# Performance work log

Hardware: AMD Instinct MI355X
Metric: run time of the kernel (lower is better)

The kernel has to match this reference:

```python
import jax, jax.numpy as jnp
import numpy as np

BETA = 0.25
N_EMBED = 1024
DIM = 256


def setup_inputs() -> dict:
    key = jax.random.key(0)
    k1, k2 = jax.random.split(key)
    z = jax.random.normal(k1, (8, DIM, 64, 64), dtype=jnp.float32)
    # matches nn.Embedding init: uniform(-1/n_embed, 1/n_embed)
    codebook = jax.random.uniform(
        k2, (N_EMBED, DIM), dtype=jnp.float32,
        minval=-1.0 / N_EMBED, maxval=1.0 / N_EMBED)
    return {"z": z, "codebook": codebook}


def reference(z, codebook):
    B, C, H, W = z.shape
    sg = jax.lax.stop_gradient
    zp = jnp.transpose(z, (0, 2, 3, 1))          # [B,H,W,C]
    zf = zp.reshape(-1, C)                        # [N,C], N = B*H*W
    # squared euclidean distances: ||z||^2 + ||e||^2 - 2 z.e
    d = (jnp.sum(zf * zf, axis=1, keepdims=True)
         + jnp.sum(codebook * codebook, axis=1)
         - 2.0 * zf @ codebook.T)                 # [N, n_embed]
    idx = jnp.argmin(d, axis=1)                   # [N]
    # one-hot @ codebook in the original is just an index gather
    z_q = codebook[idx].reshape(zp.shape)         # [B,H,W,C]
    loss = (BETA * jnp.mean((sg(z_q) - zp) ** 2)
            + jnp.mean((z_q - sg(zp)) ** 2))
    z_q_st = zp + sg(z_q - zp)                    # straight-through estimator
    z_q_out = jnp.transpose(z_q_st, (0, 3, 1, 2))  # back to NCHW
    return z_q_out, loss, idx.reshape(B, H, W)
```

## Files before the change

### kernel.cpp

```cpp
#include <hip/hip_runtime.h>
#include <hip/hip_fp16.h>

#define NELEM 8388608
#define M_GAP 6e-4f
#define SCORE_SCALE (-1.0f / 512.0f)

typedef _Float16 f16x8 __attribute__((ext_vector_type(8)));
typedef short s16x8 __attribute__((ext_vector_type(8)));
typedef float f32x4 __attribute__((ext_vector_type(4)));

__device__ __forceinline__ unsigned short bf16r(float f) {
  unsigned u = __float_as_uint(f);
  return (unsigned short)((u + 0x7fffu + ((u >> 16) & 1u)) >> 16);
}
__device__ __forceinline__ float bf16f(unsigned short h) {
  return __uint_as_float(((unsigned)h) << 16);
}

__device__ __forceinline__ float pw128_sq(const float* p, int s) {
  float r[8];
#pragma unroll
  for (int j = 0; j < 8; ++j) { float v = p[j * s]; r[j] = __fmul_rn(v, v); }
#pragma unroll
  for (int i = 8; i < 128; i += 8) {
#pragma unroll
    for (int j = 0; j < 8; ++j) {
      float v = p[(i + j) * s];
      r[j] = __fadd_rn(r[j], __fmul_rn(v, v));
    }
  }
  return __fadd_rn(__fadd_rn(__fadd_rn(r[0], r[1]), __fadd_rn(r[2], r[3])),
                   __fadd_rn(__fadd_rn(r[4], r[5]), __fadd_rn(r[6], r[7])));
}
__device__ __forceinline__ float np_sumsq256(const float* p, int s) {
  return __fadd_rn(pw128_sq(p, s), pw128_sq(p + 128 * s, s));
}

__global__ __launch_bounds__(256)
void vq_prep(const float* __restrict__ cb, unsigned short* __restrict__ cbimg,
             float* __restrict__ cbT, float* __restrict__ Bsg,
             unsigned* __restrict__ cnt, float* __restrict__ loss) {
  int gid = blockIdx.x * 256 + threadIdx.x;
  if (gid == 0) { *cnt = 0u; *loss = 0.0f; }
  int j = gid >> 2, qt = gid & 3;
  const float4* row4 = reinterpret_cast<const float4*>(cb + (size_t)j * 256 + qt * 64);
  int T = j >> 4, jj = j & 15;
#pragma unroll
  for (int m8 = 0; m8 < 8; ++m8) {
    int c0 = qt * 64 + m8 * 8;
    int kk = c0 >> 5, lk = (c0 >> 3) & 3;
    float4 va = row4[m8 * 2];
    float4 vb = row4[m8 * 2 + 1];
    float v[8] = {va.x, va.y, va.z, va.w, vb.x, vb.y, vb.z, vb.w};
    s16x8 hv;
#pragma unroll
    for (int q = 0; q < 8; ++q) {
      hv[q] = (short)__half_as_ushort(__float2half(v[q] * 1024.0f));
      cbT[(size_t)(c0 + q) * 1024 + j] = v[q];
    }
    *reinterpret_cast<s16x8*>(cbimg + (size_t)T * 4096 + kk * 512 + (lk * 16 + jj) * 8) = hv;
  }
  if (qt == 0) Bsg[j] = np_sumsq256(cb + (size_t)j * 256, 1);
}

#define VQ_STEP_PF(IT2, DO_PF)                                                 \
  {                                                                            \
    f32x4 acc[4];                                                              \
    _Pragma("unroll")                                                          \
    for (int rs = 0; rs < 4; ++rs) acc[rs] = (f32x4){0.f, 0.f, 0.f, 0.f};      \
    _Pragma("unroll")                                                          \
    for (int kk = 0; kk < 8; ++kk) {                                           \
      f16x8 bcur = ba[kk];                                                     \
      if (DO_PF)                                                               \
        ba[kk] = cimg2[(size_t)(wv * 16 + (IT2) + 1) * 512 + kk * 64 + lane];  \
      _Pragma("unroll")                                                        \
      for (int rs = 0; rs < 4; ++rs)                                           \
        acc[rs] = __builtin_amdgcn_mfma_f32_16x16x32_f16(ah[rs][kk], bcur,     \
                                                         acc[rs], 0, 0, 0);    \
    }                                                                          \
    int j = wv * 256 + (IT2) * 16 + l15;                                       \
    float Bj = BsL[j];                                                         \
    _Pragma("unroll")                                                          \
    for (int rs = 0; rs < 4; ++rs) {                                           \
      _Pragma("unroll")                                                        \
      for (int r = 0; r < 4; ++r) {                                            \
        float s = fmaf(SCORE_SCALE, acc[rs][r], Bj);                           \
        bool lt = s < b1v[rs][r];                                              \
        float other = lt ? b1v[rs][r] : s;                                     \
        b2v[rs][r] = fminf(b2v[rs][r], other);                                 \
        b1v[rs][r] = fminf(b1v[rs][r], s);                                     \
        b1i[rs][r] = lt ? j : b1i[rs][r];                                      \
      }                                                                        \
    }                                                                          \
  }

__global__ __launch_bounds__(256, 1)
void vq_fast(const float* __restrict__ z, const float* __restrict__ cb,
             const unsigned short* __restrict__ cbimg,
             const float* __restrict__ Bsg,
             float* __restrict__ zq, float* __restrict__ loss,
             float* __restrict__ idxo,
             unsigned* __restrict__ list, unsigned* __restrict__ cnt,
             float* __restrict__ zdump) {
  __shared__ __align__(16) unsigned char buf[58880];
  __shared__ float BsL[1024];
  __shared__ float part[32][36];
  __shared__ float rowA[64];
  __shared__ int bestj[64];
  __shared__ float bestd[64];
  __shared__ unsigned char flg[64];
  __shared__ float wred[4];
  __shared__ float cv1[4 * 64], cv2[4 * 64];
  __shared__ int ci1[4 * 64];

  const int t = threadIdx.x;
  const int bid = blockIdx.x;
  const int lane = t & 63;
  const int wv = t >> 6;
  const int l15 = lane & 15;
  const int lk = lane >> 4;

  const f16x8* cimg2 = reinterpret_cast<const f16x8*>(cbimg);
  float* zt = reinterpret_cast<float*>(buf);
  const float4* z4 = reinterpret_cast<const float4*>(
      z + (size_t)(bid >> 6) * 1048576 + (size_t)(bid & 63) * 64);

  f16x8 ba[8];
#pragma unroll
  for (int kk = 0; kk < 8; ++kk)
    ba[kk] = cimg2[(size_t)(wv * 16) * 512 + kk * 64 + lane];

  for (int i = t; i < 1024; i += 256) BsL[i] = Bsg[i];

  f16x8 ah[4][8];
#pragma unroll
  for (int hp = 0; hp < 2; ++hp) {
    float sq[4] = {0.f, 0.f, 0.f, 0.f};
#pragma unroll
    for (int i = 0; i < 8; ++i) {
      int idx = t + i * 256;
      int c = idx >> 3, w4p = idx & 7;
      float4 v = z4[(size_t)c * 1024 + hp * 8 + w4p];
      zt[c * 33 + w4p * 4 + 0] = v.x;
      zt[c * 33 + w4p * 4 + 1] = v.y;
      zt[c * 33 + w4p * 4 + 2] = v.z;
      zt[c * 33 + w4p * 4 + 3] = v.w;
      sq[0] += v.x * v.x; sq[1] += v.y * v.y;
      sq[2] += v.z * v.z; sq[3] += v.w * v.w;
    }
#pragma unroll
    for (int q = 0; q < 4; ++q) part[t >> 3][(t & 7) * 4 + q] = sq[q];
    __syncthreads();
    if (t < 32) {
      float s = 0.f;
#pragma unroll
      for (int g = 0; g < 32; ++g) s += part[g][t];
      rowA[hp * 32 + t] = s;
    }
#pragma unroll
    for (int rr2 = 0; rr2 < 2; ++rr2) {
      int lr = rr2 * 16 + l15;
#pragma unroll
      for (int kk = 0; kk < 8; ++kk)
#pragma unroll
        for (int m = 0; m < 8; ++m)
          ah[hp * 2 + rr2][kk][m] = (_Float16)zt[(kk * 32 + lk * 8 + m) * 33 + lr];
    }
    if (zdump) {
#pragma unroll
      for (int i = 0; i < 8; ++i) {
        int item = t + i * 256;
        int c4 = item & 63, rowp = item >> 6;
        float4 v = make_float4(zt[(c4 * 4 + 0) * 33 + rowp],
                               zt[(c4 * 4 + 1) * 33 + rowp],
                               zt[(c4 * 4 + 2) * 33 + rowp],
                               zt[(c4 * 4 + 3) * 33 + rowp]);
        *reinterpret_cast<float4*>(
            zdump + ((size_t)bid * 64 + hp * 32 + rowp) * 256 + c4 * 4) = v;
      }
    }
    __syncthreads();
  }

  float b1v[4][4], b2v[4][4];
  int b1i[4][4];
#pragma unroll
  for (int rs = 0; rs < 4; ++rs)
#pragma unroll
    for (int r = 0; r < 4; ++r) { b1v[rs][r] = 3.4e38f; b2v[rs][r] = 3.4e38f; b1i[rs][r] = 0; }

  for (int it = 0; it < 15; ++it) {
    VQ_STEP_PF(it, true);
  }
  VQ_STEP_PF(15, false);

#pragma unroll
  for (int mk = 1; mk < 16; mk <<= 1) {
#pragma unroll
    for (int rs = 0; rs < 4; ++rs)
#pragma unroll
      for (int r = 0; r < 4; ++r) {
        float ov1 = __shfl_xor(b1v[rs][r], mk, 64);
        float ov2 = __shfl_xor(b2v[rs][r], mk, 64);
        int oi1 = __shfl_xor(b1i[rs][r], mk, 64);
        bool lt = ov1 < b1v[rs][r];
        float hi = lt ? b1v[rs][r] : ov1;
        b2v[rs][r] = fminf(fminf(b2v[rs][r], ov2), hi);
        b1v[rs][r] = fminf(b1v[rs][r], ov1);
        b1i[rs][r] = lt ? oi1 : b1i[rs][r];
      }
  }
  if (l15 == 0) {
#pragma unroll
    for (int rs = 0; rs < 4; ++rs)
#pragma unroll
      for (int r = 0; r < 4; ++r) {
        int rr = rs * 16 + lk * 4 + r;
        cv1[wv * 64 + rr] = b1v[rs][r];
        cv2[wv * 64 + rr] = b2v[rs][r];
        ci1[wv * 64 + rr] = b1i[rs][r];
      }
  }
  __syncthreads();

  if (t < 64) {
    float v1 = cv1[t], v2 = cv2[t];
    int i1 = ci1[t];
#pragma unroll
    for (int w = 1; w < 4; ++w) {
      float u1 = cv1[w * 64 + t], u2 = cv2[w * 64 + t];
      int ui = ci1[w * 64 + t];
      if (u1 < v1) { v2 = fminf(v1, u2); v1 = u1; i1 = ui; }
      else v2 = fminf(v2, u1);
    }
    bestj[t] = i1;
    bestd[t] = v1;
    flg[t] = (v2 - v1 <= M_GAP) ? 1 : 0;
    int n = bid * 64 + t;
    idxo[n] = (float)i1;
    if (flg[t]) { unsigned pos = atomicAdd(cnt, 1u); list[pos] = (unsigned)n; }
  }
  __syncthreads();

  {
    float lv = (t < 64) ? (rowA[t] + bestd[t]) : 0.f;
#pragma unroll
    for (int off = 32; off > 0; off >>= 1) lv += __shfl_down(lv, off, 64);
    if (lane == 0) wred[wv] = lv;
  }
  __syncthreads();
  if (t == 0)
    atomicAdd(loss, (wred[0] + wred[1] + wred[2] + wred[3]) * (1.25f / (float)NELEM));

  f32x4* ldsF4 = reinterpret_cast<f32x4*>(buf);
  const float* ldsF = reinterpret_cast<const float*>(buf);
  const float4* cb4 = reinterpret_cast<const float4*>(cb);
  float* zqb = zq + (size_t)(bid >> 6) * 1048576 + (size_t)(bid & 63) * 64;
  for (int hp = 0; hp < 2; ++hp) {
    __syncthreads();
#pragma unroll
    for (int i = 0; i < 8; ++i) {
      int item = t + i * 256;
      int rr = item >> 6, cc = item & 63;
      float4 v = cb4[(size_t)bestj[hp * 32 + rr] * 64 + cc];
      ldsF4[rr * 64 + (cc ^ ((rr >> 2) & 7))] = (f32x4){v.x, v.y, v.z, v.w};
    }
    __syncthreads();
#pragma unroll
    for (int i = 0; i < 8; ++i) {
      int item = t + i * 256;
      int w4p = item & 7, c = item >> 3;
      float ov[4];
#pragma unroll
      for (int q = 0; q < 4; ++q) {
        int rr = w4p * 4 + q;
        ov[q] = ldsF[(rr * 64 + ((c >> 2) ^ ((rr >> 2) & 7))) * 4 + (c & 3)];
      }
      *reinterpret_cast<float4*>(zqb + (size_t)c * 4096 + hp * 32 + w4p * 4) =
          make_float4(ov[0], ov[1], ov[2], ov[3]);
    }
  }
}

__global__ __launch_bounds__(256)
void vq_exact_fast(const float* __restrict__ zdump, const float* __restrict__ cbT,
                   const float* __restrict__ Bsg, const unsigned* __restrict__ list,
                   const unsigned* __restrict__ cnt, float* __restrict__ idxo) {
  __shared__ float zr[8][260];
  __shared__ float Anp[8];
  __shared__ float rv[256];
  __shared__ int ri[256];
  const int t = threadIdx.x;
  const unsigned K = *cnt;
  const float4* cbT4 = reinterpret_cast<const float4*>(cbT);
  const float4* zd4 = reinterpret_cast<const float4*>(zdump);

  for (unsigned g = blockIdx.x; g * 8 < K; g += gridDim.x) {
    int nrows = (int)min(8u, K - g * 8);
    __syncthreads();
#pragma unroll
    for (int i = 0; i < 2; ++i) {
      int idx = t + i * 256;
      int r = idx >> 6, c4 = idx & 63;
      if (r < nrows) {
        float4 v = zd4[(size_t)list[g * 8 + r] * 64 + c4];
        zr[r][c4 * 4 + 0] = v.x; zr[r][c4 * 4 + 1] = v.y;
        zr[r][c4 * 4 + 2] = v.z; zr[r][c4 * 4 + 3] = v.w;
      }
    }
    __syncthreads();
    if (t < nrows) Anp[t] = np_sumsq256(&zr[t][0], 1);
    __syncthreads();

    float acc[8][4];
#pragma unroll
    for (int r = 0; r < 8; ++r)
#pragma unroll
      for (int q = 0; q < 4; ++q) acc[r][q] = 0.f;
    for (int c = 0; c < 256; ++c) {
      float4 bv = cbT4[c * 256 + t];
#pragma unroll
      for (int r = 0; r < 8; ++r) {
        float zc = zr[r][c];
        acc[r][0] = fmaf(zc, bv.x, acc[r][0]);
        acc[r][1] = fmaf(zc, bv.y, acc[r][1]);
        acc[r][2] = fmaf(zc, bv.z, acc[r][2]);
        acc[r][3] = fmaf(zc, bv.w, acc[r][3]);
      }
    }
    for (int r = 0; r < nrows; ++r) {
      float A = Anp[r];
      float bvv = 3.4e38f;
      int bii = 0;
#pragma unroll
      for (int q = 0; q < 4; ++q) {
        int j = t * 4 + q;
        float dd = __fsub_rn(__fadd_rn(A, Bsg[j]), __fmul_rn(2.0f, acc[r][q]));
        if (dd < bvv) { bvv = dd; bii = j; }
      }
      rv[t] = bvv; ri[t] = bii;
      __syncthreads();
      for (int s2 = 128; s2 > 0; s2 >>= 1) {
        if (t < s2) {
          float v2 = rv[t + s2]; int i2 = ri[t + s2];
          if (v2 < rv[t] || (v2 == rv[t] && i2 < ri[t])) { rv[t] = v2; ri[t] = i2; }
        }
        __syncthreads();
      }
      if (t == 0) idxo[list[g * 8 + r]] = (float)ri[0];
      __syncthreads();
    }
  }
}

__global__ __launch_bounds__(256)
void vq_exact_scatter(const float* __restrict__ z, const float* __restrict__ cbT,
                      const float* __restrict__ Bsg, const unsigned* __restrict__ list,
                      const unsigned* __restrict__ cnt, float* __restrict__ idxo) {
  __shared__ float zr[8][260];
  __shared__ float Anp[8];
  __shared__ float rv[256];
  __shared__ int ri[256];
  const int t = threadIdx.x;
  const unsigned K = *cnt;
  const float4* cbT4 = reinterpret_cast<const float4*>(cbT);

  for (unsigned g = blockIdx.x; g * 8 < K; g += gridDim.x) {
    int nrows = (int)min(8u, K - g * 8);
    __syncthreads();
    {
      int r = t >> 5, l32 = t & 31;
      if (r < nrows) {
        int n = (int)list[g * 8 + r];
        int b = n >> 12, hw = n & 4095;
        const float* zb = z + (size_t)b * 1048576 + hw;
#pragma unroll
        for (int q = 0; q < 8; ++q) {
          int c = l32 * 8 + q;
          zr[r][c] = zb[(size_t)c * 4096];
        }
      }
    }
    __syncthreads();
    if (t < nrows) Anp[t] = np_sumsq256(&zr[t][0], 1);
    __syncthreads();
    float acc[8][4];
#pragma unroll
    for (int r = 0; r < 8; ++r)
#pragma unroll
      for (int q = 0; q < 4; ++q) acc[r][q] = 0.f;
    for (int c = 0; c < 256; ++c) {
      float4 bv = cbT4[c * 256 + t];
#pragma unroll
      for (int r = 0; r < 8; ++r) {
        float zc = zr[r][c];
        acc[r][0] = fmaf(zc, bv.x, acc[r][0]);
        acc[r][1] = fmaf(zc, bv.y, acc[r][1]);
        acc[r][2] = fmaf(zc, bv.z, acc[r][2]);
        acc[r][3] = fmaf(zc, bv.w, acc[r][3]);
      }
    }
    for (int r = 0; r < nrows; ++r) {
      float A = Anp[r];
      float bvv = 3.4e38f;
      int bii = 0;
#pragma unroll
      for (int q = 0; q < 4; ++q) {
        int j = t * 4 + q;
        float dd = __fsub_rn(__fadd_rn(A, Bsg[j]), __fmul_rn(2.0f, acc[r][q]));
        if (dd < bvv) { bvv = dd; bii = j; }
      }
      rv[t] = bvv; ri[t] = bii;
      __syncthreads();
      for (int s2 = 128; s2 > 0; s2 >>= 1) {
        if (t < s2) {
          float v2 = rv[t + s2]; int i2 = ri[t + s2];
          if (v2 < rv[t] || (v2 == rv[t] && i2 < ri[t])) { rv[t] = v2; ri[t] = i2; }
        }
        __syncthreads();
      }
      if (t == 0) idxo[list[g * 8 + r]] = (float)ri[0];
      __syncthreads();
    }
  }
}

__global__ __launch_bounds__(256)
void vq_ref(const float* __restrict__ z, const float* __restrict__ cb,
            float* __restrict__ zq, float* __restrict__ loss,
            float* __restrict__ idxo) {
  __shared__ __align__(16) float zt[256 * 64];
  __shared__ __align__(16) float cbt[256 * 64];
  __shared__ float As[64];
  __shared__ float Bs[64];
  __shared__ int bestj[64];
  __shared__ float cand_v[16 * 64];
  __shared__ int cand_i[16 * 64];
  __shared__ double wred[4];
  const int t = threadIdx.x;
  const int wg = t & 15, jg = t >> 4;
  const int bid = blockIdx.x;
  const int b = bid >> 6, h = bid & 63;
  const int n0 = bid * 64;
  const float4* z4 = reinterpret_cast<const float4*>(z + (size_t)b * 256 * 4096 + (size_t)h * 64);
  float4* zt4 = reinterpret_cast<float4*>(zt);
#pragma unroll
  for (int i = 0; i < 16; ++i) {
    int idx4 = t + i * 256;
    zt4[idx4] = z4[(size_t)(idx4 >> 4) * 1024 + (idx4 & 15)];
  }
  __syncthreads();
  if (t < 64) As[t] = np_sumsq256(zt + t, 64);
  float bv[4]; int bi[4];
#pragma unroll
  for (int a = 0; a < 4; ++a) { bv[a] = 3.4e38f; bi[a] = 0; }
  for (int p = 0; p < 16; ++p) {
    __syncthreads();
    const float4* cb4 = reinterpret_cast<const float4*>(cb) + (size_t)p * 64 * 64;
#pragma unroll
    for (int i = 0; i < 16; ++i) {
      int idx4 = t + i * 256;
      int jj = idx4 >> 6, c4 = idx4 & 63;
      float4 v = cb4[idx4];
      cbt[(c4 * 4 + 0) * 64 + jj] = v.x;
      cbt[(c4 * 4 + 1) * 64 + jj] = v.y;
      cbt[(c4 * 4 + 2) * 64 + jj] = v.z;
      cbt[(c4 * 4 + 3) * 64 + jj] = v.w;
    }
    __syncthreads();
    if (t < 64) Bs[t] = np_sumsq256(cbt + t, 64);
    float acc[4][4];
#pragma unroll
    for (int a = 0; a < 4; ++a)
#pragma unroll
      for (int u = 0; u < 4; ++u) acc[a][u] = 0.0f;
    const float4* ztp = reinterpret_cast<const float4*>(zt) + wg;
    const float4* cbp = reinterpret_cast<const float4*>(cbt) + jg;
#pragma unroll 4
    for (int c = 0; c < 256; ++c) {
      float4 zv = ztp[c * 16];
      float4 cv = cbp[c * 16];
      float za[4] = {zv.x, zv.y, zv.z, zv.w};
      float ca[4] = {cv.x, cv.y, cv.z, cv.w};
#pragma unroll
      for (int a = 0; a < 4; ++a)
#pragma unroll
        for (int u = 0; u < 4; ++u) acc[a][u] = fmaf(za[a], ca[u], acc[a][u]);
    }
    __syncthreads();
#pragma unroll
    for (int u = 0; u < 4; ++u) {
      int j = p * 64 + jg * 4 + u;
      float Bju = Bs[jg * 4 + u];
#pragma unroll
      for (int a = 0; a < 4; ++a) {
        float AB = __fadd_rn(As[wg * 4 + a], Bju);
        float dd = __fsub_rn(AB, __fmul_rn(2.0f, acc[a][u]));
        if (dd < bv[a]) { bv[a] = dd; bi[a] = j; }
      }
    }
  }
  __syncthreads();
#pragma unroll
  for (int a = 0; a < 4; ++a) {
    int w = wg * 4 + a;
    cand_v[jg * 64 + w] = bv[a];
    cand_i[jg * 64 + w] = bi[a];
  }
  __syncthreads();
  if (t < 64) {
    float v0 = cand_v[t]; int i0 = cand_i[t];
    for (int g = 1; g < 16; ++g) {
      float v = cand_v[g * 64 + t]; int ii = cand_i[g * 64 + t];
      if (v < v0 || (v == v0 && ii < i0)) { v0 = v; i0 = ii; }
    }
    bestj[t] = i0;
    idxo[n0 + t] = (float)i0;
  }
  __syncthreads();
  double lsum = 0.0;
  float* zqbase = zq + (size_t)b * 256 * 4096 + (size_t)h * 64;
  for (int i = 0; i < 64; ++i) {
    int idx = t + i * 256;
    int c = idx >> 6, w = idx & 63;
    float zvv = zt[c * 64 + w];
    float cvv = cb[(size_t)bestj[w] * 256 + c];
    zqbase[(size_t)c * 4096 + w] = cvv;
    double d = (double)cvv - (double)zvv;
    lsum += d * d;
  }
#pragma unroll
  for (int off = 32; off > 0; off >>= 1) lsum += __shfl_down(lsum, off, 64);
  if ((t & 63) == 0) wred[t >> 6] = lsum;
  __syncthreads();
  if (t == 0) {
    double tot = wred[0] + wred[1] + wred[2] + wred[3];
    atomicAdd(loss, (float)(tot * (1.25 / (double)NELEM)));
  }
}

extern "C" void kernel_launch(void* const* d_in, const int* in_sizes, int n_in,
                              void* d_out, int out_size, void* d_ws, size_t ws_size,
                              hipStream_t stream) {
  (void)in_sizes; (void)n_in; (void)out_size;
  const float* z = (const float*)d_in[0];
  const float* cb = (const float*)d_in[1];
  float* out = (float*)d_out;
  float* zq = out;
  float* loss = out + NELEM;
  float* idxo = out + NELEM + 1;
  if (ws_size < 1712128) {
    hipMemsetAsync(loss, 0, sizeof(float), stream);
    vq_ref<<<512, 256, 0, stream>>>(z, cb, zq, loss, idxo);
    return;
  }
  unsigned char* ws = (unsigned char*)d_ws;
  unsigned* cnt = (unsigned*)ws;
  float* Bsg = (float*)(ws + 1024);
  unsigned* list = (unsigned*)(ws + 8192);
  float* cbT = (float*)(ws + 139264);
  unsigned short* cbimg = (unsigned short*)(ws + 1187840);
  const bool have_dump = (ws_size >= 35651584);
  float* zdump = have_dump ? (float*)(ws + 2097152) : nullptr;
  vq_prep<<<16, 256, 0, stream>>>(cb, cbimg, cbT, Bsg, cnt, loss);
  vq_fast<<<512, 256, 0, stream>>>(z, cb, cbimg, Bsg, zq, loss, idxo, list, cnt, zdump);
  if (have_dump)
    vq_exact_fast<<<512, 256, 0, stream>>>(zdump, cbT, Bsg, list, cnt, idxo);
  else
    vq_exact_scatter<<<512, 256, 0, stream>>>(z, cbT, Bsg, list, cnt, idxo);
}
```

Measured before the change: 104.0 us.

## Track top-3 scores to resolve near-ties with a cheap two-candidate check

The fast fp16 MFMA pass now keeps the best three scores and the top two indices per row. Ambiguous rows whose third-best is clearly separated go to a new per-thread kernel that recomputes only the two candidate distances in fp32. Only rows with three-way near ties fall back to the full exact rescan over all 1024 codes. The scatter fallback is removed, the z dump is always written, and the smaller-workspace path now uses the reference kernel. The extra compare logic and registers in the hot loop may cost occupancy or issue slots, and there is one more kernel launch.

```diff
diff --git a/kernel.cpp b/kernel.cpp
--- a/kernel.cpp
+++ b/kernel.cpp
@@ -41,7 +41,7 @@
              float* __restrict__ cbT, float* __restrict__ Bsg,
              unsigned* __restrict__ cnt, float* __restrict__ loss) {
   int gid = blockIdx.x * 256 + threadIdx.x;
-  if (gid == 0) { *cnt = 0u; *loss = 0.0f; }
+  if (gid == 0) { cnt[0] = 0u; cnt[1] = 0u; *loss = 0.0f; }
   int j = gid >> 2, qt = gid & 3;
   const float4* row4 = reinterpret_cast<const float4*>(cb + (size_t)j * 256 + qt * 64);
   int T = j >> 4, jj = j & 15;
@@ -85,11 +85,14 @@
       _Pragma("unroll")                                                        \
       for (int r = 0; r < 4; ++r) {                                            \
         float s = fmaf(SCORE_SCALE, acc[rs][r], Bj);                           \
-        bool lt = s < b1v[rs][r];                                              \
-        float other = lt ? b1v[rs][r] : s;                                     \
-        b2v[rs][r] = fminf(b2v[rs][r], other);                                 \
-        b1v[rs][r] = fminf(b1v[rs][r], s);                                     \
-        b1i[rs][r] = lt ? j : b1i[rs][r];                                      \
+        bool lt1 = s < b1v[rs][r];                                             \
+        bool lt2 = s < b2v[rs][r];                                             \
+        bool lt3 = s < b3v[rs][r];                                             \
+        b3v[rs][r] = lt2 ? b2v[rs][r] : (lt3 ? s : b3v[rs][r]);                \
+        b2v[rs][r] = lt1 ? b1v[rs][r] : (lt2 ? s : b2v[rs][r]);                \
+        b2i[rs][r] = lt1 ? b1i[rs][r] : (lt2 ? j : b2i[rs][r]);                \
+        b1v[rs][r] = lt1 ? s : b1v[rs][r];                                     \
+        b1i[rs][r] = lt1 ? j : b1i[rs][r];                                     \
       }                                                                        \
     }                                                                          \
   }
@@ -100,7 +103,8 @@
              const float* __restrict__ Bsg,
              float* __restrict__ zq, float* __restrict__ loss,
              float* __restrict__ idxo,
-             unsigned* __restrict__ list, unsigned* __restrict__ cnt,
+             unsigned* __restrict__ plist, unsigned* __restrict__ pcand,
+             unsigned* __restrict__ flist, unsigned* __restrict__ cnt,
              float* __restrict__ zdump) {
   __shared__ __align__(16) unsigned char buf[58880];
   __shared__ float BsL[1024];
@@ -108,10 +112,9 @@
   __shared__ float rowA[64];
   __shared__ int bestj[64];
   __shared__ float bestd[64];
-  __shared__ unsigned char flg[64];
   __shared__ float wred[4];
-  __shared__ float cv1[4 * 64], cv2[4 * 64];
-  __shared__ int ci1[4 * 64];
+  __shared__ float cv1[4 * 64], cv2[4 * 64], cv3[4 * 64];
+  __shared__ int ci1[4 * 64], ci2[4 * 64];
 
   const int t = threadIdx.x;
   const int bid = blockIdx.x;
@@ -166,28 +169,29 @@
         for (int m = 0; m < 8; ++m)
           ah[hp * 2 + rr2][kk][m] = (_Float16)zt[(kk * 32 + lk * 8 + m) * 33 + lr];
     }
-    if (zdump) {
-#pragma unroll
-      for (int i = 0; i < 8; ++i) {
-        int item = t + i * 256;
-        int c4 = item & 63, rowp = item >> 6;
-        float4 v = make_float4(zt[(c4 * 4 + 0) * 33 + rowp],
-                               zt[(c4 * 4 + 1) * 33 + rowp],
-                               zt[(c4 * 4 + 2) * 33 + rowp],
-                               zt[(c4 * 4 + 3) * 33 + rowp]);
-        *reinterpret_cast<float4*>(
-            zdump + ((size_t)bid * 64 + hp * 32 + rowp) * 256 + c4 * 4) = v;
-      }
-    }
-    __syncthreads();
-  }
-
-  float b1v[4][4], b2v[4][4];
-  int b1i[4][4];
+#pragma unroll
+    for (int i = 0; i < 8; ++i) {
+      int item = t + i * 256;
+      int c4 = item & 63, rowp = item >> 6;
+      float4 v = make_float4(zt[(c4 * 4 + 0) * 33 + rowp],
+                             zt[(c4 * 4 + 1) * 33 + rowp],
+                             zt[(c4 * 4 + 2) * 33 + rowp],
+                             zt[(c4 * 4 + 3) * 33 + rowp]);
+      *reinterpret_cast<float4*>(
+          zdump + ((size_t)bid * 64 + hp * 32 + rowp) * 256 + c4 * 4) = v;
+    }
+    __syncthreads();
+  }
+
+  float b1v[4][4], b2v[4][4], b3v[4][4];
+  int b1i[4][4], b2i[4][4];
 #pragma unroll
   for (int rs = 0; rs < 4; ++rs)
 #pragma unroll
-    for (int r = 0; r < 4; ++r) { b1v[rs][r] = 3.4e38f; b2v[rs][r] = 3.4e38f; b1i[rs][r] = 0; }
+    for (int r = 0; r < 4; ++r) {
+      b1v[rs][r] = 3.4e38f; b2v[rs][r] = 3.4e38f; b3v[rs][r] = 3.4e38f;
+      b1i[rs][r] = 0; b2i[rs][r] = 0;
+    }
 
   for (int it = 0; it < 15; ++it) {
     VQ_STEP_PF(it, true);
@@ -202,12 +206,22 @@
       for (int r = 0; r < 4; ++r) {
         float ov1 = __shfl_xor(b1v[rs][r], mk, 64);
         float ov2 = __shfl_xor(b2v[rs][r], mk, 64);
+        float ov3 = __shfl_xor(b3v[rs][r], mk, 64);
         int oi1 = __shfl_xor(b1i[rs][r], mk, 64);
-        bool lt = ov1 < b1v[rs][r];
-        float hi = lt ? b1v[rs][r] : ov1;
-        b2v[rs][r] = fminf(fminf(b2v[rs][r], ov2), hi);
-        b1v[rs][r] = fminf(b1v[rs][r], ov1);
-        b1i[rs][r] = lt ? oi1 : b1i[rs][r];
+        int oi2 = __shfl_xor(b2i[rs][r], mk, 64);
+        bool bw = ov1 < b1v[rs][r];
+        float w2 = bw ? ov2 : b2v[rs][r];
+        int wi2 = bw ? oi2 : b2i[rs][r];
+        float w3 = bw ? ov3 : b3v[rs][r];
+        float l1 = bw ? b1v[rs][r] : ov1;
+        int li1 = bw ? b1i[rs][r] : oi1;
+        float l2 = bw ? b2v[rs][r] : ov2;
+        b1v[rs][r] = bw ? ov1 : b1v[rs][r];
+        b1i[rs][r] = bw ? oi1 : b1i[rs][r];
+        bool sw = w2 < l1;
+        b2v[rs][r] = sw ? w2 : l1;
+        b2i[rs][r] = sw ? wi2 : li1;
+        b3v[rs][r] = sw ? fminf(w3, l1) : fminf(w2, l2);
       }
   }
   if (l15 == 0) {
@@ -218,27 +232,44 @@
         int rr = rs * 16 + lk * 4 + r;
         cv1[wv * 64 + rr] = b1v[rs][r];
         cv2[wv * 64 + rr] = b2v[rs][r];
+        cv3[wv * 64 + rr] = b3v[rs][r];
         ci1[wv * 64 + rr] = b1i[rs][r];
+        ci2[wv * 64 + rr] = b2i[rs][r];
       }
   }
   __syncthreads();
 
   if (t < 64) {
-    float v1 = cv1[t], v2 = cv2[t];
-    int i1 = ci1[t];
+    float v1 = cv1[t], v2 = cv2[t], v3 = cv3[t];
+    int i1 = ci1[t], i2 = ci2[t];
 #pragma unroll
     for (int w = 1; w < 4; ++w) {
-      float u1 = cv1[w * 64 + t], u2 = cv2[w * 64 + t];
-      int ui = ci1[w * 64 + t];
-      if (u1 < v1) { v2 = fminf(v1, u2); v1 = u1; i1 = ui; }
-      else v2 = fminf(v2, u1);
+      float u1 = cv1[w * 64 + t], u2 = cv2[w * 64 + t], u3 = cv3[w * 64 + t];
+      int ui1 = ci1[w * 64 + t], ui2 = ci2[w * 64 + t];
+      bool bw = u1 < v1;
+      float w2 = bw ? u2 : v2;  int wi2 = bw ? ui2 : i2;
+      float w3 = bw ? u3 : v3;
+      float l1 = bw ? v1 : u1;  int li1 = bw ? i1 : ui1;
+      float l2 = bw ? v2 : u2;
+      v1 = bw ? u1 : v1;  i1 = bw ? ui1 : i1;
+      bool sw = w2 < l1;
+      v2 = sw ? w2 : l1;  i2 = sw ? wi2 : li1;
+      v3 = sw ? fminf(w3, l1) : fminf(w2, l2);
     }
     bestj[t] = i1;
     bestd[t] = v1;
-    flg[t] = (v2 - v1 <= M_GAP) ? 1 : 0;
     int n = bid * 64 + t;
     idxo[n] = (float)i1;
-    if (flg[t]) { unsigned pos = atomicAdd(cnt, 1u); list[pos] = (unsigned)n; }
+    if (v2 - v1 <= M_GAP) {
+      if (v3 - v1 > M_GAP) {
+        unsigned pos = atomicAdd(&cnt[0], 1u);
+        plist[pos] = (unsigned)n;
+        pcand[pos] = (unsigned)i1 | ((unsigned)i2 << 16);
+      } else {
+        unsigned pos = atomicAdd(&cnt[1], 1u);
+        flist[pos] = (unsigned)n;
+      }
+    }
   }
   __syncthreads();
 
@@ -279,6 +310,34 @@
       *reinterpret_cast<float4*>(zqb + (size_t)c * 4096 + hp * 32 + w4p * 4) =
           make_float4(ov[0], ov[1], ov[2], ov[3]);
     }
+  }
+}
+
+__global__ __launch_bounds__(256)
+void vq_pair(const float* __restrict__ zdump, const float* __restrict__ cb,
+             const float* __restrict__ Bsg, const unsigned* __restrict__ plist,
+             const unsigned* __restrict__ pcand, const unsigned* __restrict__ cnt,
+             float* __restrict__ idxo) {
+  const unsigned K = cnt[0];
+  for (unsigned idx = blockIdx.x * 256 + threadIdx.x; idx < K;
+       idx += gridDim.x * 256) {
+    int n = (int)plist[idx];
+    unsigned pk = pcand[idx];
+    int j1 = (int)(pk & 0xffffu), j2 = (int)(pk >> 16);
+    const float* zr = zdump + (size_t)n * 256;
+    const float* c1 = cb + (size_t)j1 * 256;
+    const float* c2 = cb + (size_t)j2 * 256;
+    float A = np_sumsq256(zr, 1);
+    float C1 = 0.f, C2 = 0.f;
+    for (int c = 0; c < 256; ++c) {
+      float zc = zr[c];
+      C1 = fmaf(zc, c1[c], C1);
+      C2 = fmaf(zc, c2[c], C2);
+    }
+    float d1 = __fsub_rn(__fadd_rn(A, Bsg[j1]), __fmul_rn(2.0f, C1));
+    float d2 = __fsub_rn(__fadd_rn(A, Bsg[j2]), __fmul_rn(2.0f, C2));
+    int win = (d2 < d1 || (d2 == d1 && j2 < j1)) ? j2 : j1;
+    idxo[n] = (float)win;
   }
 }
 
@@ -312,78 +371,6 @@
     if (t < nrows) Anp[t] = np_sumsq256(&zr[t][0], 1);
     __syncthreads();
 
-    float acc[8][4];
-#pragma unroll
-    for (int r = 0; r < 8; ++r)
-#pragma unroll
-      for (int q = 0; q < 4; ++q) acc[r][q] = 0.f;
-    for (int c = 0; c < 256; ++c) {
-      float4 bv = cbT4[c * 256 + t];
-#pragma unroll
-      for (int r = 0; r < 8; ++r) {
-        float zc = zr[r][c];
-        acc[r][0] = fmaf(zc, bv.x, acc[r][0]);
-        acc[r][1] = fmaf(zc, bv.y, acc[r][1]);
-        acc[r][2] = fmaf(zc, bv.z, acc[r][2]);
-        acc[r][3] = fmaf(zc, bv.w, acc[r][3]);
-      }
-    }
-    for (int r = 0; r < nrows; ++r) {
-      float A = Anp[r];
-      float bvv = 3.4e38f;
-      int bii = 0;
-#pragma unroll
-      for (int q = 0; q < 4; ++q) {
-        int j = t * 4 + q;
-        float dd = __fsub_rn(__fadd_rn(A, Bsg[j]), __fmul_rn(2.0f, acc[r][q]));
-        if (dd < bvv) { bvv = dd; bii = j; }
-      }
-      rv[t] = bvv; ri[t] = bii;
-      __syncthreads();
-      for (int s2 = 128; s2 > 0; s2 >>= 1) {
-        if (t < s2) {
-          float v2 = rv[t + s2]; int i2 = ri[t + s2];
-          if (v2 < rv[t] || (v2 == rv[t] && i2 < ri[t])) { rv[t] = v2; ri[t] = i2; }
-        }
-        __syncthreads();
-      }
-      if (t == 0) idxo[list[g * 8 + r]] = (float)ri[0];
-      __syncthreads();
-    }
-  }
-}
-
-__global__ __launch_bounds__(256)
-void vq_exact_scatter(const float* __restrict__ z, const float* __restrict__ cbT,
-                      const float* __restrict__ Bsg, const unsigned* __restrict__ list,
-                      const unsigned* __restrict__ cnt, float* __restrict__ idxo) {
-  __shared__ float zr[8][260];
-  __shared__ float Anp[8];
-  __shared__ float rv[256];
-  __shared__ int ri[256];
-  const int t = threadIdx.x;
-  const unsigned K = *cnt;
-  const float4* cbT4 = reinterpret_cast<const float4*>(cbT);
-
-  for (unsigned g = blockIdx.x; g * 8 < K; g += gridDim.x) {
-    int nrows = (int)min(8u, K - g * 8);
-    __syncthreads();
-    {
-      int r = t >> 5, l32 = t & 31;
-      if (r < nrows) {
-        int n = (int)list[g * 8 + r];
-        int b = n >> 12, hw = n & 4095;
-        const float* zb = z + (size_t)b * 1048576 + hw;
-#pragma unroll
-        for (int q = 0; q < 8; ++q) {
-          int c = l32 * 8 + q;
-          zr[r][c] = zb[(size_t)c * 4096];
-        }
-      }
-    }
-    __syncthreads();
-    if (t < nrows) Anp[t] = np_sumsq256(&zr[t][0], 1);
-    __syncthreads();
     float acc[8][4];
 #pragma unroll
     for (int r = 0; r < 8; ++r)
@@ -549,7 +536,7 @@
   float* zq = out;
   float* loss = out + NELEM;
   float* idxo = out + NELEM + 1;
-  if (ws_size < 1712128) {
+  if (ws_size < 35651584) {
     hipMemsetAsync(loss, 0, sizeof(float), stream);
     vq_ref<<<512, 256, 0, stream>>>(z, cb, zq, loss, idxo);
     return;
@@ -557,15 +544,15 @@
   unsigned char* ws = (unsigned char*)d_ws;
   unsigned* cnt = (unsigned*)ws;
   float* Bsg = (float*)(ws + 1024);
-  unsigned* list = (unsigned*)(ws + 8192);
-  float* cbT = (float*)(ws + 139264);
-  unsigned short* cbimg = (unsigned short*)(ws + 1187840);
-  const bool have_dump = (ws_size >= 35651584);
-  float* zdump = have_dump ? (float*)(ws + 2097152) : nullptr;
+  unsigned* plist = (unsigned*)(ws + 8192);
+  unsigned* pcand = (unsigned*)(ws + 139264);
+  unsigned* flist = (unsigned*)(ws + 270336);
+  float* cbT = (float*)(ws + 401408);
+  unsigned short* cbimg = (unsigned short*)(ws + 1449984);
+  float* zdump = (float*)(ws + 2097152);
   vq_prep<<<16, 256, 0, stream>>>(cb, cbimg, cbT, Bsg, cnt, loss);
-  vq_fast<<<512, 256, 0, stream>>>(z, cb, cbimg, Bsg, zq, loss, idxo, list, cnt, zdump);
-  if (have_dump)
-    vq_exact_fast<<<512, 256, 0, stream>>>(zdump, cbT, Bsg, list, cnt, idxo);
-  else
-    vq_exact_scatter<<<512, 256, 0, stream>>>(z, cbT, Bsg, list, cnt, idxo);
-}
+  vq_fast<<<512, 256, 0, stream>>>(z, cb, cbimg, Bsg, zq, loss, idxo,
+                                   plist, pcand, flist, cnt, zdump);
+  vq_pair<<<64, 256, 0, stream>>>(zdump, cb, Bsg, plist, pcand, cnt, idxo);
+  vq_exact_fast<<<64, 256, 0, stream>>>(zdump, cbT, Bsg, flist, cnt + 1, idxo);
+}
```

Measured after the change: 147.1 us. 1.41x slower.
